# Kernel tuning notes

Hardware: AMD Instinct MI355X
Metric: run time of the kernel (lower is better)

## Reference

```python
import jax, jax.numpy as jnp
import numpy as np

N_NODES = 100000
N_EDGES = 1600000
EPS = 1e-5  # nn.BatchNorm1d default eps


def setup_inputs() -> dict:
    key = jax.random.key(0)
    ks = jax.random.split(key, 6)
    x = jax.random.normal(ks[0], (N_NODES, 11), dtype=jnp.float32)
    edge_index = jax.random.randint(ks[1], (2, N_EDGES), 0, N_NODES, dtype=jnp.int64)
    edge_weight = jax.random.uniform(ks[2], (N_EDGES,), dtype=jnp.float32)
    W1 = jax.random.normal(ks[3], (11, 64), dtype=jnp.float32) * 0.3
    b1 = jnp.zeros((64,), dtype=jnp.float32)
    gamma = jnp.ones((64,), dtype=jnp.float32)
    beta = jnp.zeros((64,), dtype=jnp.float32)
    W2 = jax.random.normal(ks[4], (64, 128), dtype=jnp.float32) * 0.125
    b2 = jnp.zeros((128,), dtype=jnp.float32)
    return {"x": x, "edge_index": edge_index, "edge_weight": edge_weight,
            "W1": W1, "b1": b1, "gamma": gamma, "beta": beta, "W2": W2, "b2": b2}


def _gcn_conv(x, row, col, w, W, b, n_nodes):
    """PyG GCNConv: h = x @ W; symmetric-norm aggregate at col; + bias.
    row/col/w already include self loops (weight 1.0)."""
    h = x @ W  # [N, F_out]
    deg = jax.ops.segment_sum(w, col, num_segments=n_nodes)  # [N]
    dinv = jnp.where(deg > 0, jax.lax.rsqrt(jnp.maximum(deg, 1e-12)), 0.0)
    norm = dinv[row] * w * dinv[col]  # [E+N]
    msg = h[row] * norm[:, None]  # gather + scale, [E+N, F_out]
    out = jax.ops.segment_sum(msg, col, num_segments=n_nodes)  # scatter-add
    return out + b


def _batch_norm(x, gamma, beta):
    # training-mode BatchNorm1d over node dimension, biased variance
    mean = jnp.mean(x, axis=0)
    var = jnp.mean(jnp.square(x - mean), axis=0)
    return (x - mean) * jax.lax.rsqrt(var + EPS) * gamma + beta


def reference(x, edge_index, edge_weight, W1, b1, gamma, beta, W2, b2):
    n = x.shape[0]
    loops = jnp.arange(n, dtype=edge_index.dtype)
    row = jnp.concatenate([edge_index[0], loops])
    col = jnp.concatenate([edge_index[1], loops])
    w = jnp.concatenate([edge_weight, jnp.ones((n,), dtype=edge_weight.dtype)])

    h = _gcn_conv(x, row, col, w, W1, b1, n)
    h = _batch_norm(h, gamma, beta)
    h = jax.nn.relu(h)
    # dropout is identity at inference (deterministic baseline)
    out = _gcn_conv(h, row, col, w, W2, b2, n)
    return out
```

## Files before the change

kernel.cpp:

```cpp
#include <hip/hip_runtime.h>

#define F0 11
#define F1 64
#define F2 128
#define TN2 128

#define CHUNKS 64
#define BPR 12544
#define WPR (BPR / 2)
#define NBKT (CHUNKS * 8 * 4)
#define NN1 64

__device__ __forceinline__ unsigned short f2bf(float v) {
  unsigned u = __float_as_uint(v);
  unsigned r = u + 0x7FFFu + ((u >> 16) & 1u);
  return (unsigned short)(r >> 16);
}
__device__ __forceinline__ float bf2f(unsigned short s) {
  return __uint_as_float(((unsigned)s) << 16);
}
__device__ __forceinline__ float bf2f_lo(unsigned v) { return __uint_as_float(v << 16); }
__device__ __forceinline__ float bf2f_hi(unsigned v) { return __uint_as_float(v & 0xFFFF0000u); }

__global__ void k_pad(const float* __restrict__ x, unsigned short* __restrict__ x16b, int n) {
  int i = blockIdx.x * blockDim.x + threadIdx.x;
  if (i >= n * 16) return;
  int r = i >> 4, f = i & 15;
  x16b[i] = (f < F0) ? f2bf(x[(size_t)r * F0 + f]) : (unsigned short)0;
}

__global__ __launch_bounds__(1024) void k_cnt8(const int* __restrict__ col,
                                               int* __restrict__ bcnt, int E, int CE) {
  __shared__ int scnt[16][8];
  int bid = blockIdx.x;
  int c = bid >> 2, q = bid & 3;
  int e0 = c * CE, e1 = min(E, e0 + CE);
  int S = (CE + 3) >> 2;
  int s0 = e0 + q * S, s1 = min(e1, s0 + S);
  int t = threadIdx.x, wv = t >> 6, lane = t & 63;
  int cr[8] = {0, 0, 0, 0, 0, 0, 0, 0};
  for (int e = s0 + t; e < s1; e += 1024) {
    int r = col[e] / BPR;
#pragma unroll
    for (int rr = 0; rr < 8; rr++) cr[rr] += (r == rr) ? 1 : 0;
  }
#pragma unroll
  for (int rr = 0; rr < 8; rr++) {
    int v = cr[rr];
#pragma unroll
    for (int d = 32; d > 0; d >>= 1) v += __shfl_down(v, d);
    if (lane == 0) scnt[wv][rr] = v;
  }
  __syncthreads();
  if (t < 8) {
    int s = 0;
    for (int i = 0; i < 16; i++) s += scnt[i][t];
    bcnt[(c * 8 + t) * 4 + q] = s;
  }
}

__global__ void k_scan8(const int* __restrict__ bcnt, int* __restrict__ boff) {
  __shared__ int s[1024];
  int t = threadIdx.x;
  int v0 = bcnt[2 * t], v1 = bcnt[2 * t + 1];
  int pv = v0 + v1;
  s[t] = pv;
  __syncthreads();
  for (int d = 1; d < 1024; d <<= 1) {
    int x = (t >= d) ? s[t - d] : 0;
    __syncthreads();
    s[t] += x;
    __syncthreads();
  }
  int ex = s[t] - pv;
  boff[2 * t] = ex;
  boff[2 * t + 1] = ex + v0;
  if (t == 1023) boff[2048] = s[1023];
}

__global__ __launch_bounds__(1024) void k_scatter(const int* __restrict__ col,
                                                  const int* __restrict__ row,
                                                  const float* __restrict__ w,
                                                  const int* __restrict__ boff,
                                                  unsigned short* __restrict__ bloc,
                                                  uint2* __restrict__ brw, int E, int CE) {
  __shared__ int cur[8];
  int bid = blockIdx.x;
  int c = bid >> 2, q = bid & 3;
  int t = threadIdx.x;
  if (t < 8) cur[t] = boff[(c * 8 + t) * 4 + q];
  __syncthreads();
  int e0 = c * CE, e1 = min(E, e0 + CE);
  int S = (CE + 3) >> 2;
  int s0 = e0 + q * S, s1 = min(e1, s0 + S);
  for (int e = s0 + t; e < s1; e += 1024) {
    int b = col[e];
    int r = b / BPR;
    int pos = atomicAdd(&cur[r], 1);
    bloc[pos] = (unsigned short)(b - r * BPR);
    brw[pos] = make_uint2((unsigned)row[e], __float_as_uint(w[e]));
  }
}

__global__ __launch_bounds__(1024) void k_hist2(const unsigned short* __restrict__ bloc,
                                                const int* __restrict__ boff,
                                                unsigned* __restrict__ partial, int ranges) {
  __shared__ unsigned lds[WPR];
  int r = blockIdx.x % ranges;
  int c = blockIdx.x / ranges;
  int t = threadIdx.x;
  for (int i = t; i < WPR; i += 1024) lds[i] = 0;
  __syncthreads();
  int s0 = boff[(c * 8 + r) * 4], s1 = boff[(c * 8 + r) * 4 + 4];
  for (int i = s0 + t; i < s1; i += 1024) {
    int local = bloc[i];
    atomicAdd(&lds[local >> 1], 1u << (16 * (local & 1)));
  }
  __syncthreads();
  unsigned* dst = partial + ((size_t)r * CHUNKS + c) * WPR;
  for (int i = t; i < WPR; i += 1024) dst[i] = lds[i];
}

__global__ void k_colprefix(const unsigned* __restrict__ partial,
                            unsigned short* __restrict__ rel,
                            int* __restrict__ cnt, int N, int npad) {
  int bin = blockIdx.x * blockDim.x + threadIdx.x;
  if (bin >= N) return;
  int r = bin / BPR, local = bin % BPR;
  int word = local >> 1, sh = 16 * (local & 1);
  const unsigned* p = partial + (size_t)r * CHUNKS * WPR + word;
  unsigned acc = 0;
  for (int c = 0; c < CHUNKS; c++) {
    unsigned v = (p[(size_t)c * WPR] >> sh) & 0xFFFFu;
    rel[(size_t)c * npad + bin] = (unsigned short)acc;
    acc += v;
  }
  cnt[bin] = (int)acc;
}

__global__ void k_scan1(const int* __restrict__ cnt, int* __restrict__ offs,
                        int* __restrict__ bsum, int n) {
  __shared__ int s[1024];
  int tid = threadIdx.x;
  int i = blockIdx.x * 1024 + tid;
  int v = (i < n) ? cnt[i] : 0;
  s[tid] = v;
  __syncthreads();
  for (int d = 1; d < 1024; d <<= 1) {
    int t = (tid >= d) ? s[tid - d] : 0;
    __syncthreads();
    s[tid] += t;
    __syncthreads();
  }
  if (i < n) offs[i] = s[tid] - v;
  if (tid == 1023) bsum[blockIdx.x] = s[1023];
}

__global__ void k_scan2(int* __restrict__ bsum, int nb) {
  __shared__ int s[256];
  __shared__ int carry;
  int t = threadIdx.x;
  if (t == 0) carry = 0;
  __syncthreads();
  for (int base = 0; base < nb; base += 256) {
    int v = (base + t < nb) ? bsum[base + t] : 0;
    s[t] = v;
    __syncthreads();
    for (int d = 1; d < 256; d <<= 1) {
      int x = (t >= d) ? s[t - d] : 0;
      __syncthreads();
      s[t] += x;
      __syncthreads();
    }
    int total = s[255];
    if (base + t < nb) bsum[base + t] = carry + s[t] - v;
    __syncthreads();
    if (t == 0) carry += total;
    __syncthreads();
  }
}

__global__ void k_scan3(int* __restrict__ offs, const int* __restrict__ bsum,
                        int n, int total) {
  int i = blockIdx.x * 1024 + threadIdx.x;
  if (i < n) offs[i] += bsum[blockIdx.x];
  if (i == 0) offs[n] = total;
}

__global__ __launch_bounds__(1024) void k_fill2(const unsigned short* __restrict__ bloc,
                                                const uint2* __restrict__ brw,
                                                const int* __restrict__ boff,
                                                const int* __restrict__ offs,
                                                const unsigned short* __restrict__ rel,
                                                uint2* __restrict__ csr8,
                                                int N, int npad, int ranges) {
  __shared__ unsigned cur[WPR];
  int r = blockIdx.x % ranges;
  int c = blockIdx.x / ranges;
  int lo = r * BPR;
  int hi = min(N, lo + BPR);
  int t = threadIdx.x;
  const unsigned* rsrc = (const unsigned*)(rel + (size_t)c * npad + lo);
  int nw = (hi - lo + 1) >> 1;
  for (int i = t; i < nw; i += 1024) cur[i] = rsrc[i];
  __syncthreads();
  int s0 = boff[(c * 8 + r) * 4], s1 = boff[(c * 8 + r) * 4 + 4];
  for (int i = s0 + t; i < s1; i += 1024) {
    int local = bloc[i];
    int sh = 16 * (local & 1);
    unsigned old = atomicAdd(&cur[local >> 1], 1u << sh);
    unsigned myrel = (old >> sh) & 0xFFFFu;
    int pos = offs[lo + local] + (int)myrel;
    uint2 b = brw[i];
    csr8[pos] = make_uint2(b.x | ((unsigned)local << 17), b.y);
  }
}

__global__ void k_deg2(const uint2* __restrict__ csr8, const int* __restrict__ offs,
                       float* __restrict__ dinv, int n) {
  int wid = (blockIdx.x * blockDim.x + threadIdx.x) >> 6;
  int lane = threadIdx.x & 63;
  if (wid >= n) return;
  int s = offs[wid], e = offs[wid + 1];
  float acc = 0.f;
  for (int k = s + lane; k < e; k += 64) acc += __uint_as_float(csr8[k].y);
#pragma unroll
  for (int d = 32; d > 0; d >>= 1) acc += __shfl_down(acc, d);
  if (lane == 0) dinv[wid] = rsqrtf(1.0f + acc);
}

__global__ void k_norm(uint2* __restrict__ csr8, const float* __restrict__ dinv, int E) {
  int i = blockIdx.x * blockDim.x + threadIdx.x;
  if (i >= E) return;
  uint2 v = csr8[i];
  csr8[i].y = __float_as_uint(dinv[v.x & 0x1FFFFu] * __uint_as_float(v.y));
}

__global__ __launch_bounds__(256) void k_agg1e(const unsigned short* __restrict__ x16b,
                                               const int* __restrict__ offs,
                                               const uint2* __restrict__ csr8,
                                               const float* __restrict__ dinv,
                                               const float* __restrict__ W1,
                                               const float* __restrict__ b1,
                                               unsigned short* __restrict__ h,
                                               float2* __restrict__ pbn, int N) {
  __shared__ float Ws[F0 * F1];
  __shared__ float bs[F1];
  __shared__ float sacc[NN1 * 16];
  __shared__ unsigned short sx[NN1 * 16];
  __shared__ float sdinv[NN1];
  __shared__ float sS[4][64], sQ[4][64];
  int t = threadIdx.x;
  int bid = blockIdx.x;
  int n0 = bid * NN1;
  int nn = min(NN1, N - n0);
  int lbase = n0 - (n0 / BPR) * BPR;
  for (int i = t; i < F0 * F1; i += 256) Ws[i] = W1[i];
  if (t < F1) bs[t] = b1[t];
  ((uint2*)sx)[t] = ((const uint2*)(x16b + (size_t)n0 * 16))[t];
  if (t < NN1) sdinv[t] = (t < nn) ? dinv[n0 + t] : 0.f;
  for (int i = t; i < NN1 * 16; i += 256) sacc[i] = 0.f;
  __syncthreads();
  int ebase = offs[n0], eend = offs[n0 + nn];
  int slot = t >> 4, f = t & 15;
  int nsub = (eend - ebase + 15) >> 4;
  int gs = ebase + slot * nsub;
  int ge = min(eend, gs + nsub);
  float sum = 0.f;
  int cid = -1;
  int e = gs;
  for (; e + 4 <= ge; e += 4) {
    uint2 v0 = csr8[e], v1 = csr8[e + 1], v2 = csr8[e + 2], v3 = csr8[e + 3];
    int i0 = (int)(v0.x >> 17) - lbase, i1 = (int)(v1.x >> 17) - lbase;
    int i2 = (int)(v2.x >> 17) - lbase, i3 = (int)(v3.x >> 17) - lbase;
    float c0 = __uint_as_float(v0.y) * bf2f(x16b[(size_t)(v0.x & 0x1FFFFu) * 16 + f]);
    float c1 = __uint_as_float(v1.y) * bf2f(x16b[(size_t)(v1.x & 0x1FFFFu) * 16 + f]);
    float c2 = __uint_as_float(v2.y) * bf2f(x16b[(size_t)(v2.x & 0x1FFFFu) * 16 + f]);
    float c3 = __uint_as_float(v3.y) * bf2f(x16b[(size_t)(v3.x & 0x1FFFFu) * 16 + f]);
    bool sm;
    sm = (i0 == cid); if (!sm && cid >= 0) atomicAdd(&sacc[cid * 16 + f], sum);
    sum = sm ? sum + c0 : c0; cid = i0;
    sm = (i1 == cid); if (!sm) atomicAdd(&sacc[cid * 16 + f], sum);
    sum = sm ? sum + c1 : c1; cid = i1;
    sm = (i2 == cid); if (!sm) atomicAdd(&sacc[cid * 16 + f], sum);
    sum = sm ? sum + c2 : c2; cid = i2;
    sm = (i3 == cid); if (!sm) atomicAdd(&sacc[cid * 16 + f], sum);
    sum = sm ? sum + c3 : c3; cid = i3;
  }
  for (; e < ge; e++) {
    uint2 v0 = csr8[e];
    int i0 = (int)(v0.x >> 17) - lbase;
    float c0 = __uint_as_float(v0.y) * bf2f(x16b[(size_t)(v0.x & 0x1FFFFu) * 16 + f]);
    bool sm = (i0 == cid);
    if (!sm && cid >= 0) atomicAdd(&sacc[cid * 16 + f], sum);
    sum = sm ? sum + c0 : c0; cid = i0;
  }
  if (cid >= 0) atomicAdd(&sacc[cid * 16 + f], sum);
  __syncthreads();
  for (int i = t; i < NN1 * 16; i += 256) {
    float di = sdinv[i >> 4];
    sacc[i] = di * (sacc[i] + di * bf2f(sx[i]));
  }
  __syncthreads();
  int ff = t & 63, wv = t >> 6;
  float S = 0.f, Q = 0.f;
  for (int i = 0; i < 16; i++) {
    int nd = wv + 4 * i;
    if (nd < nn) {
      float o = bs[ff];
#pragma unroll
      for (int k = 0; k < F0; k++) o += sacc[nd * 16 + k] * Ws[k * F1 + ff];
      h[(size_t)(n0 + nd) * F1 + ff] = f2bf(o);
      S += o; Q += o * o;
    }
  }
  sS[wv][ff] = S; sQ[wv][ff] = Q;
  __syncthreads();
  if (t < 64)
    pbn[(size_t)bid * 64 + t] =
        make_float2(sS[0][t] + sS[1][t] + sS[2][t] + sS[3][t],
                    sQ[0][t] + sQ[1][t] + sQ[2][t] + sQ[3][t]);
}

__global__ void k_bn_mid(const float2* __restrict__ pbn, float2* __restrict__ pbn2, int nrows) {
  __shared__ float sS[4][64], sQ[4][64];
  int t = threadIdx.x;
  int f = t & 63, g = t >> 6;
  int rpb = (nrows + 63) / 64;
  int b0 = blockIdx.x * rpb;
  int bend = min(nrows, b0 + rpb);
  float S = 0.f, Q = 0.f;
  for (int b = b0 + g; b < bend; b += 4) {
    float2 v = pbn[(size_t)b * 64 + f];
    S += v.x; Q += v.y;
  }
  sS[g][f] = S; sQ[g][f] = Q;
  __syncthreads();
  if (t < 64)
    pbn2[(size_t)blockIdx.x * 64 + t] =
        make_float2(sS[0][t] + sS[1][t] + sS[2][t] + sS[3][t],
                    sQ[0][t] + sQ[1][t] + sQ[2][t] + sQ[3][t]);
}

__global__ void k_bn_final(const float2* __restrict__ pbn2, const float* __restrict__ gamma,
                           const float* __restrict__ beta, float* __restrict__ scalef,
                           float* __restrict__ shiftf, int n) {
  __shared__ double sS[4][64], sQ[4][64];
  int t = threadIdx.x;
  int f = t & 63, g = t >> 6;
  double S = 0.0, Q = 0.0;
  for (int b = g; b < 64; b += 4) {
    float2 v = pbn2[(size_t)b * 64 + f];
    S += v.x; Q += v.y;
  }
  sS[g][f] = S; sQ[g][f] = Q;
  __syncthreads();
  if (t < 64) {
    double SS = sS[0][t] + sS[1][t] + sS[2][t] + sS[3][t];
    double QQ = sQ[0][t] + sQ[1][t] + sQ[2][t] + sQ[3][t];
    double mean = SS / (double)n;
    double var = QQ / (double)n - mean * mean;
    if (var < 0.0) var = 0.0;
    float scale = gamma[t] * (float)(1.0 / sqrt(var + 1e-5));
    scalef[t] = scale;
    shiftf[t] = beta[t] - (float)mean * scale;
  }
}

__global__ void k_hn(const unsigned short* __restrict__ h, const float* __restrict__ scalef,
                     const float* __restrict__ shiftf, unsigned short* __restrict__ hn,
                     int total4) {
  __shared__ float ssc[64], ssf[64];
  int t = threadIdx.x;
  if (t < 64) { ssc[t] = scalef[t]; ssf[t] = shiftf[t]; }
  __syncthreads();
  int idx = blockIdx.x * blockDim.x + t;
  int stride = gridDim.x * blockDim.x;
  const unsigned long long* hp = (const unsigned long long*)h;
  unsigned long long* hnp = (unsigned long long*)hn;
  for (int i = idx; i < total4; i += stride) {
    unsigned long long vv = hp[i];
    int f0 = (i * 4) & 63;
    float a = fmaxf(fmaf(bf2f_lo((unsigned)vv), ssc[f0 + 0], ssf[f0 + 0]), 0.f);
    float b = fmaxf(fmaf(bf2f_hi((unsigned)vv), ssc[f0 + 1], ssf[f0 + 1]), 0.f);
    float c = fmaxf(fmaf(bf2f_lo((unsigned)(vv >> 32)), ssc[f0 + 2], ssf[f0 + 2]), 0.f);
    float d = fmaxf(fmaf(bf2f_hi((unsigned)(vv >> 32)), ssc[f0 + 3], ssf[f0 + 3]), 0.f);
    hnp[i] = (unsigned long long)f2bf(a) | ((unsigned long long)f2bf(b) << 16) |
             ((unsigned long long)f2bf(c) << 32) | ((unsigned long long)f2bf(d) << 48);
  }
}

__global__ void k_agg2(const unsigned short* __restrict__ hn, const int* __restrict__ offs,
                       const uint2* __restrict__ csr8, const float* __restrict__ dinv,
                       float* __restrict__ agg2, int n) {
  __shared__ unsigned s_soff[4][64];
  __shared__ float    s_nrm[4][64];
  int t = threadIdx.x;
  int wv = t >> 6;
  int lane = t & 63;
  int wid = (blockIdx.x * blockDim.x + t) >> 6;
  if (wid >= n) return;
  float di = dinv[wid];
  float a0 = di * bf2f(hn[(size_t)wid * F1 + lane]);
  float a1 = 0.f, a2 = 0.f, a3 = 0.f, a4 = 0.f, a5 = 0.f, a6 = 0.f, a7 = 0.f;
  int s = offs[wid], e = offs[wid + 1];
  for (int base = s; base < e; base += 64) {
    int m = e - base; if (m > 64) m = 64;
    if (lane < m) {
      uint2 v = csr8[base + lane];
      s_soff[wv][lane] = (v.x & 0x1FFFFu) * 64u;
      s_nrm[wv][lane] = __uint_as_float(v.y);
    } else {
      s_soff[wv][lane] = 0u;
      s_nrm[wv][lane] = 0.f;
    }
    int mp = (m + 7) & ~7;
    for (int j = 0; j < mp; j += 8) {
      unsigned o0 = s_soff[wv][j + 0], o1 = s_soff[wv][j + 1];
      unsigned o2 = s_soff[wv][j + 2], o3 = s_soff[wv][j + 3];
      unsigned o4 = s_soff[wv][j + 4], o5 = s_soff[wv][j + 5];
      unsigned o6 = s_soff[wv][j + 6], o7 = s_soff[wv][j + 7];
      float m0 = s_nrm[wv][j + 0], m1 = s_nrm[wv][j + 1];
      float m2 = s_nrm[wv][j + 2], m3 = s_nrm[wv][j + 3];
      float m4 = s_nrm[wv][j + 4], m5 = s_nrm[wv][j + 5];
      float m6 = s_nrm[wv][j + 6], m7 = s_nrm[wv][j + 7];
      a0 += m0 * bf2f(hn[(size_t)o0 + lane]);
      a1 += m1 * bf2f(hn[(size_t)o1 + lane]);
      a2 += m2 * bf2f(hn[(size_t)o2 + lane]);
      a3 += m3 * bf2f(hn[(size_t)o3 + lane]);
      a4 += m4 * bf2f(hn[(size_t)o4 + lane]);
      a5 += m5 * bf2f(hn[(size_t)o5 + lane]);
      a6 += m6 * bf2f(hn[(size_t)o6 + lane]);
      a7 += m7 * bf2f(hn[(size_t)o7 + lane]);
    }
  }
  agg2[(size_t)wid * F1 + lane] =
      di * (((a0 + a1) + (a2 + a3)) + ((a4 + a5) + (a6 + a7)));
}

__global__ __launch_bounds__(256) void k_gemm2(const float* __restrict__ agg2,
                                               const float* __restrict__ W2,
                                               const float* __restrict__ b2,
                                               float* __restrict__ out, int n) {
  __shared__ float Ws[F1 * F2];
  __shared__ float As[F1][TN2];
  int t = threadIdx.x;
  for (int i = t; i < F1 * F2 / 4; i += 256) ((float4*)Ws)[i] = ((const float4*)W2)[i];
  int nb = blockIdx.x * TN2;
  int node = t & 127;
  int kh = (t >> 7) * 32;
  int gnode = nb + node;
  if (gnode < n) {
    const float4* src = (const float4*)(agg2 + (size_t)gnode * F1 + kh);
#pragma unroll
    for (int j = 0; j < 8; j++) {
      float4 v = src[j];
      As[kh + j * 4 + 0][node] = v.x;
      As[kh + j * 4 + 1][node] = v.y;
      As[kh + j * 4 + 2][node] = v.z;
      As[kh + j * 4 + 3][node] = v.w;
    }
  } else {
#pragma unroll
    for (int j = 0; j < 8; j++) {
      As[kh + j * 4 + 0][node] = 0.f;
      As[kh + j * 4 + 1][node] = 0.f;
      As[kh + j * 4 + 2][node] = 0.f;
      As[kh + j * 4 + 3][node] = 0.f;
    }
  }
  __syncthreads();

  int f0 = (t & 15) * 8;
  int n0 = (t >> 4) * 8;
  float acc[8][8];
  float bv[8];
#pragma unroll
  for (int j = 0; j < 8; j++) bv[j] = b2[f0 + j];
#pragma unroll
  for (int i = 0; i < 8; i++)
#pragma unroll
    for (int j = 0; j < 8; j++) acc[i][j] = bv[j];

#pragma unroll 4
  for (int k = 0; k < F1; k++) {
    float4 a0 = *(const float4*)&As[k][n0];
    float4 a1 = *(const float4*)&As[k][n0 + 4];
    float4 w0 = *(const float4*)&Ws[k * F2 + f0];
    float4 w1 = *(const float4*)&Ws[k * F2 + f0 + 4];
    float a[8] = {a0.x, a0.y, a0.z, a0.w, a1.x, a1.y, a1.z, a1.w};
    float w[8] = {w0.x, w0.y, w0.z, w0.w, w1.x, w1.y, w1.z, w1.w};
#pragma unroll
    for (int i = 0; i < 8; i++)
#pragma unroll
      for (int j = 0; j < 8; j++) acc[i][j] += a[i] * w[j];
  }

#pragma unroll
  for (int i = 0; i < 8; i++) {
    int gi = nb + n0 + i;
    if (gi < n) {
      float4 o0 = {acc[i][0], acc[i][1], acc[i][2], acc[i][3]};
      float4 o1 = {acc[i][4], acc[i][5], acc[i][6], acc[i][7]};
      *(float4*)&out[(size_t)gi * F2 + f0] = o0;
      *(float4*)&out[(size_t)gi * F2 + f0 + 4] = o1;
    }
  }
}

extern "C" void kernel_launch(void* const* d_in, const int* in_sizes, int n_in,
                              void* d_out, int out_size, void* d_ws, size_t ws_size,
                              hipStream_t stream) {
  const float* x     = (const float*)d_in[0];
  const int*   ei    = (const int*)d_in[1];
  const float* ew    = (const float*)d_in[2];
  const float* W1    = (const float*)d_in[3];
  const float* b1    = (const float*)d_in[4];
  const float* gamma = (const float*)d_in[5];
  const float* beta  = (const float*)d_in[6];
  const float* W2    = (const float*)d_in[7];
  const float* b2    = (const float*)d_in[8];
  float* out = (float*)d_out;

  int N = in_sizes[0] / F0;
  int E = in_sizes[1] / 2;
  const int* row = ei;
  const int* col = ei + E;
  if (N <= 0) return;

  int CE = (E + CHUNKS - 1) / CHUNKS;
  int RANGES = (N + BPR - 1) / BPR;
  int npad = RANGES * BPR;
  int NBLK = (N + NN1 - 1) / NN1;

  char* p = (char*)d_ws;
  auto alloc = [&](size_t bytes) -> void* {
    void* r = (void*)p;
    p += (bytes + 255) & ~(size_t)255;
    return r;
  };
  size_t partial_bytes = ((size_t)RANGES * CHUNKS * WPR * 4 + 255) & ~(size_t)255;
  size_t rel_bytes     = (size_t)CHUNKS * npad * 2;
  size_t h_bytes       = (size_t)N * F1 * 2;
  size_t region_bytes  = partial_bytes + rel_bytes;
  if (h_bytes > region_bytes) region_bytes = h_bytes;

  float*          dinv    = (float*)alloc((size_t)N * 4);
  int*            cnt     = (int*)alloc((size_t)N * 4);
  int*            offs    = (int*)alloc((size_t)(N + 1) * 4);
  int             NB      = (N + 1023) / 1024;
  int*            bsum    = (int*)alloc((size_t)NB * 4);
  uint2*          csr8    = (uint2*)alloc((size_t)E * 8);
  char*           region  = (char*)alloc(region_bytes);
  unsigned*       partial = (unsigned*)region;
  unsigned short* rel     = (unsigned short*)(region + partial_bytes);
  unsigned short* h       = (unsigned short*)region;
  unsigned short* x16b    = (unsigned short*)alloc((size_t)N * 16 * 2);
  unsigned short* hn      = (unsigned short*)alloc((size_t)N * F1 * 2);
  float*          agg2    = (float*)alloc((size_t)N * F1 * 4);
  float2*         pbn     = (float2*)alloc((size_t)NBLK * 64 * 8);
  float2*         pbn2    = (float2*)alloc((size_t)64 * 64 * 8);
  float*          scalef  = (float*)alloc(64 * 4);
  float*          shiftf  = (float*)alloc(64 * 4);
  int*            bcnt    = (int*)alloc((size_t)NBKT * 4);
  int*            boff    = (int*)alloc((size_t)(NBKT + 1) * 4);
  size_t bloc_bytes = (((size_t)E * 2) + 255) & ~(size_t)255;
  unsigned short* bloc = (unsigned short*)agg2;
  uint2*          brw  = (uint2*)((char*)agg2 + bloc_bytes);
  (void)ws_size; (void)n_in; (void)out_size;

  int bW  = (N + 3) / 4;
  int bG2 = (N + TN2 - 1) / TN2;
  int gRC = CHUNKS * RANGES;

  k_pad<<<(N * 16 + 255) / 256, 256, 0, stream>>>(x, x16b, N);
  k_cnt8<<<CHUNKS * 4, 1024, 0, stream>>>(col, bcnt, E, CE);
  k_scan8<<<1, 1024, 0, stream>>>(bcnt, boff);
  k_scatter<<<CHUNKS * 4, 1024, 0, stream>>>(col, row, ew, boff, bloc, brw, E, CE);
  k_hist2<<<gRC, 1024, 0, stream>>>(bloc, boff, partial, RANGES);
  k_colprefix<<<(N + 255) / 256, 256, 0, stream>>>(partial, rel, cnt, N, npad);
  k_scan1<<<NB, 1024, 0, stream>>>(cnt, offs, bsum, N);
  k_scan2<<<1, 256, 0, stream>>>(bsum, NB);
  k_scan3<<<NB, 1024, 0, stream>>>(offs, bsum, N, E);
  k_fill2<<<gRC, 1024, 0, stream>>>(bloc, brw, boff, offs, rel, csr8, N, npad, RANGES);
  k_deg2<<<bW, 256, 0, stream>>>(csr8, offs, dinv, N);
  k_norm<<<(E + 255) / 256, 256, 0, stream>>>(csr8, dinv, E);
  k_agg1e<<<NBLK, 256, 0, stream>>>(x16b, offs, csr8, dinv, W1, b1, h, pbn, N);
  k_bn_mid<<<64, 256, 0, stream>>>(pbn, pbn2, NBLK);
  k_bn_final<<<1, 256, 0, stream>>>(pbn2, gamma, beta, scalef, shiftf, N);
  k_hn<<<2048, 256, 0, stream>>>(h, scalef, shiftf, hn, N * F1 / 4);
  k_agg2<<<bW, 256, 0, stream>>>(hn, offs, csr8, dinv, agg2, N);
  k_gemm2<<<bG2, 256, 0, stream>>>(agg2, W2, b2, out, N);
}
```

Baseline: 214.1 us.

## Fuse degree computation into histogram and store second aggregation in bf16

Weighted in-degree is now accumulated in LDS during the histogram pass and flushed with global atomics, and dinv comes from a small elementwise kernel. The edge normalization is applied directly in the CSR fill, which removes the separate degree and normalize passes over the edge array. The agg2 intermediate is stored as bf16 and reuses the bucket scratch region, halving that traffic. The cost is float atomics, an order-dependent degree sum, and extra bf16 rounding before the final GEMM.

```diff
diff --git a/kernel.cpp b/kernel.cpp
--- a/kernel.cpp
+++ b/kernel.cpp
@@ -22,8 +22,10 @@
 __device__ __forceinline__ float bf2f_lo(unsigned v) { return __uint_as_float(v << 16); }
 __device__ __forceinline__ float bf2f_hi(unsigned v) { return __uint_as_float(v & 0xFFFF0000u); }
 
-__global__ void k_pad(const float* __restrict__ x, unsigned short* __restrict__ x16b, int n) {
+__global__ void k_pad(const float* __restrict__ x, unsigned short* __restrict__ x16b,
+                      float* __restrict__ wdeg, int n) {
   int i = blockIdx.x * blockDim.x + threadIdx.x;
+  if (i < n) wdeg[i] = 0.f;
   if (i >= n * 16) return;
   int r = i >> 4, f = i & 15;
   x16b[i] = (f < F0) ? f2bf(x[(size_t)r * F0 + f]) : (unsigned short)0;
@@ -103,22 +105,40 @@
 }
 
 __global__ __launch_bounds__(1024) void k_hist2(const unsigned short* __restrict__ bloc,
+                                                const uint2* __restrict__ brw,
                                                 const int* __restrict__ boff,
-                                                unsigned* __restrict__ partial, int ranges) {
+                                                unsigned* __restrict__ partial,
+                                                float* __restrict__ wdeg,
+                                                int N, int ranges) {
   __shared__ unsigned lds[WPR];
+  __shared__ float swdeg[BPR];
   int r = blockIdx.x % ranges;
   int c = blockIdx.x / ranges;
   int t = threadIdx.x;
   for (int i = t; i < WPR; i += 1024) lds[i] = 0;
+  for (int i = t; i < BPR; i += 1024) swdeg[i] = 0.f;
   __syncthreads();
   int s0 = boff[(c * 8 + r) * 4], s1 = boff[(c * 8 + r) * 4 + 4];
   for (int i = s0 + t; i < s1; i += 1024) {
     int local = bloc[i];
+    float wv = __uint_as_float(brw[i].y);
     atomicAdd(&lds[local >> 1], 1u << (16 * (local & 1)));
+    atomicAdd(&swdeg[local], wv);
   }
   __syncthreads();
   unsigned* dst = partial + ((size_t)r * CHUNKS + c) * WPR;
   for (int i = t; i < WPR; i += 1024) dst[i] = lds[i];
+  int lo = r * BPR;
+  int hi = min(N, lo + BPR);
+  for (int i = lo + t; i < hi; i += 1024) {
+    float v = swdeg[i - lo];
+    if (v != 0.f) atomicAdd(&wdeg[i], v);
+  }
+}
+
+__global__ void k_dinv(const float* __restrict__ wdeg, float* __restrict__ dinv, int n) {
+  int i = blockIdx.x * blockDim.x + threadIdx.x;
+  if (i < n) dinv[i] = rsqrtf(1.0f + wdeg[i]);
 }
 
 __global__ void k_colprefix(const unsigned* __restrict__ partial,
@@ -192,6 +212,7 @@
                                                 const int* __restrict__ boff,
                                                 const int* __restrict__ offs,
                                                 const unsigned short* __restrict__ rel,
+                                                const float* __restrict__ dinv,
                                                 uint2* __restrict__ csr8,
                                                 int N, int npad, int ranges) {
   __shared__ unsigned cur[WPR];
@@ -212,28 +233,9 @@
     unsigned myrel = (old >> sh) & 0xFFFFu;
     int pos = offs[lo + local] + (int)myrel;
     uint2 b = brw[i];
-    csr8[pos] = make_uint2(b.x | ((unsigned)local << 17), b.y);
-  }
-}
-
-__global__ void k_deg2(const uint2* __restrict__ csr8, const int* __restrict__ offs,
-                       float* __restrict__ dinv, int n) {
-  int wid = (blockIdx.x * blockDim.x + threadIdx.x) >> 6;
-  int lane = threadIdx.x & 63;
-  if (wid >= n) return;
-  int s = offs[wid], e = offs[wid + 1];
-  float acc = 0.f;
-  for (int k = s + lane; k < e; k += 64) acc += __uint_as_float(csr8[k].y);
-#pragma unroll
-  for (int d = 32; d > 0; d >>= 1) acc += __shfl_down(acc, d);
-  if (lane == 0) dinv[wid] = rsqrtf(1.0f + acc);
-}
-
-__global__ void k_norm(uint2* __restrict__ csr8, const float* __restrict__ dinv, int E) {
-  int i = blockIdx.x * blockDim.x + threadIdx.x;
-  if (i >= E) return;
-  uint2 v = csr8[i];
-  csr8[i].y = __float_as_uint(dinv[v.x & 0x1FFFFu] * __uint_as_float(v.y));
+    float nm = dinv[b.x] * __uint_as_float(b.y);
+    csr8[pos] = make_uint2(b.x | ((unsigned)local << 17), __float_as_uint(nm));
+  }
 }
 
 __global__ __launch_bounds__(256) void k_agg1e(const unsigned short* __restrict__ x16b,
@@ -392,7 +394,7 @@
 
 __global__ void k_agg2(const unsigned short* __restrict__ hn, const int* __restrict__ offs,
                        const uint2* __restrict__ csr8, const float* __restrict__ dinv,
-                       float* __restrict__ agg2, int n) {
+                       unsigned short* __restrict__ agg2b, int n) {
   __shared__ unsigned s_soff[4][64];
   __shared__ float    s_nrm[4][64];
   int t = threadIdx.x;
@@ -434,11 +436,11 @@
       a7 += m7 * bf2f(hn[(size_t)o7 + lane]);
     }
   }
-  agg2[(size_t)wid * F1 + lane] =
-      di * (((a0 + a1) + (a2 + a3)) + ((a4 + a5) + (a6 + a7)));
-}
-
-__global__ __launch_bounds__(256) void k_gemm2(const float* __restrict__ agg2,
+  float r = di * (((a0 + a1) + (a2 + a3)) + ((a4 + a5) + (a6 + a7)));
+  agg2b[(size_t)wid * F1 + lane] = f2bf(r);
+}
+
+__global__ __launch_bounds__(256) void k_gemm2(const unsigned short* __restrict__ agg2b,
                                                const float* __restrict__ W2,
                                                const float* __restrict__ b2,
                                                float* __restrict__ out, int n) {
@@ -451,14 +453,18 @@
   int kh = (t >> 7) * 32;
   int gnode = nb + node;
   if (gnode < n) {
-    const float4* src = (const float4*)(agg2 + (size_t)gnode * F1 + kh);
-#pragma unroll
-    for (int j = 0; j < 8; j++) {
-      float4 v = src[j];
-      As[kh + j * 4 + 0][node] = v.x;
-      As[kh + j * 4 + 1][node] = v.y;
-      As[kh + j * 4 + 2][node] = v.z;
-      As[kh + j * 4 + 3][node] = v.w;
+    const uint4* src = (const uint4*)(agg2b + (size_t)gnode * F1 + kh);
+#pragma unroll
+    for (int j = 0; j < 4; j++) {
+      uint4 v = src[j];
+      As[kh + j * 8 + 0][node] = bf2f_lo(v.x);
+      As[kh + j * 8 + 1][node] = bf2f_hi(v.x);
+      As[kh + j * 8 + 2][node] = bf2f_lo(v.y);
+      As[kh + j * 8 + 3][node] = bf2f_hi(v.y);
+      As[kh + j * 8 + 4][node] = bf2f_lo(v.z);
+      As[kh + j * 8 + 5][node] = bf2f_hi(v.z);
+      As[kh + j * 8 + 6][node] = bf2f_lo(v.w);
+      As[kh + j * 8 + 7][node] = bf2f_hi(v.w);
     }
   } else {
 #pragma unroll
@@ -546,6 +552,7 @@
   if (h_bytes > region_bytes) region_bytes = h_bytes;
 
   float*          dinv    = (float*)alloc((size_t)N * 4);
+  float*          wdeg    = (float*)alloc((size_t)N * 4);
   int*            cnt     = (int*)alloc((size_t)N * 4);
   int*            offs    = (int*)alloc((size_t)(N + 1) * 4);
   int             NB      = (N + 1023) / 1024;
@@ -557,38 +564,40 @@
   unsigned short* h       = (unsigned short*)region;
   unsigned short* x16b    = (unsigned short*)alloc((size_t)N * 16 * 2);
   unsigned short* hn      = (unsigned short*)alloc((size_t)N * F1 * 2);
-  float*          agg2    = (float*)alloc((size_t)N * F1 * 4);
+  size_t bloc_bytes = (((size_t)E * 2) + 255) & ~(size_t)255;
+  size_t bkt_bytes  = bloc_bytes + (size_t)E * 8;
+  size_t a2b_bytes  = (size_t)N * F1 * 2;
+  char*           bktreg  = (char*)alloc(bkt_bytes > a2b_bytes ? bkt_bytes : a2b_bytes);
+  unsigned short* bloc    = (unsigned short*)bktreg;
+  uint2*          brw     = (uint2*)(bktreg + bloc_bytes);
+  unsigned short* agg2b   = (unsigned short*)bktreg;
   float2*         pbn     = (float2*)alloc((size_t)NBLK * 64 * 8);
   float2*         pbn2    = (float2*)alloc((size_t)64 * 64 * 8);
   float*          scalef  = (float*)alloc(64 * 4);
   float*          shiftf  = (float*)alloc(64 * 4);
   int*            bcnt    = (int*)alloc((size_t)NBKT * 4);
   int*            boff    = (int*)alloc((size_t)(NBKT + 1) * 4);
-  size_t bloc_bytes = (((size_t)E * 2) + 255) & ~(size_t)255;
-  unsigned short* bloc = (unsigned short*)agg2;
-  uint2*          brw  = (uint2*)((char*)agg2 + bloc_bytes);
   (void)ws_size; (void)n_in; (void)out_size;
 
   int bW  = (N + 3) / 4;
   int bG2 = (N + TN2 - 1) / TN2;
   int gRC = CHUNKS * RANGES;
 
-  k_pad<<<(N * 16 + 255) / 256, 256, 0, stream>>>(x, x16b, N);
+  k_pad<<<(N * 16 + 255) / 256, 256, 0, stream>>>(x, x16b, wdeg, N);
   k_cnt8<<<CHUNKS * 4, 1024, 0, stream>>>(col, bcnt, E, CE);
   k_scan8<<<1, 1024, 0, stream>>>(bcnt, boff);
   k_scatter<<<CHUNKS * 4, 1024, 0, stream>>>(col, row, ew, boff, bloc, brw, E, CE);
-  k_hist2<<<gRC, 1024, 0, stream>>>(bloc, boff, partial, RANGES);
+  k_hist2<<<gRC, 1024, 0, stream>>>(bloc, brw, boff, partial, wdeg, N, RANGES);
+  k_dinv<<<(N + 255) / 256, 256, 0, stream>>>(wdeg, dinv, N);
   k_colprefix<<<(N + 255) / 256, 256, 0, stream>>>(partial, rel, cnt, N, npad);
   k_scan1<<<NB, 1024, 0, stream>>>(cnt, offs, bsum, N);
   k_scan2<<<1, 256, 0, stream>>>(bsum, NB);
   k_scan3<<<NB, 1024, 0, stream>>>(offs, bsum, N, E);
-  k_fill2<<<gRC, 1024, 0, stream>>>(bloc, brw, boff, offs, rel, csr8, N, npad, RANGES);
-  k_deg2<<<bW, 256, 0, stream>>>(csr8, offs, dinv, N);
-  k_norm<<<(E + 255) / 256, 256, 0, stream>>>(csr8, dinv, E);
+  k_fill2<<<gRC, 1024, 0, stream>>>(bloc, brw, boff, offs, rel, dinv, csr8, N, npad, RANGES);
   k_agg1e<<<NBLK, 256, 0, stream>>>(x16b, offs, csr8, dinv, W1, b1, h, pbn, N);
   k_bn_mid<<<64, 256, 0, stream>>>(pbn, pbn2, NBLK);
   k_bn_final<<<1, 256, 0, stream>>>(pbn2, gamma, beta, scalef, shiftf, N);
   k_hn<<<2048, 256, 0, stream>>>(h, scalef, shiftf, hn, N * F1 / 4);
-  k_agg2<<<bW, 256, 0, stream>>>(hn, offs, csr8, dinv, agg2, N);
-  k_gemm2<<<bG2, 256, 0, stream>>>(agg2, W2, b2, out, N);
-}
+  k_agg2<<<bW, 256, 0, stream>>>(hn, offs, csr8, dinv, agg2b, N);
+  k_gemm2<<<bG2, 256, 0, stream>>>(agg2b, W2, b2, out, N);
+}
```

New measurement: 212.2 us. About the same (-0.9%).
